# Kernel tuning notes

Hardware: AMD Instinct MI355X
Metric: run time of the kernel (lower is better)

The kernel has to match this reference:

```python
import jax, jax.numpy as jnp
import numpy as np

ORDER = 5
LOOKAHEAD = 0
NDF = 96  # n_df_bins


def setup_inputs() -> dict:
    key = jax.random.key(0)
    k1, k2, k3 = jax.random.split(key, 3)
    spec = jax.random.normal(k1, (16, 1, 2000, 481, 2), dtype=jnp.float32)
    coefs = jax.random.normal(k2, (16, 2000, ORDER, NDF, 2), dtype=jnp.float32)
    alpha = jax.random.uniform(k3, (16, 2000, 1), dtype=jnp.float32)
    return {"spec": spec, "coefs": coefs, "alpha": alpha}


def reference(spec, coefs, alpha):
    # spec: [B, 1, T, F, 2]; coefs: [B, T, ORDER, NDF, 2]; alpha: [B, T, 1]
    B, _, T, F, _ = spec.shape
    x = spec[:, 0, :, :NDF, :]  # [B, T, NDF, 2]
    # pad time axis: (order - lookahead - 1) before, lookahead after
    xp = jnp.pad(x, ((0, 0), (ORDER - LOOKAHEAD - 1, LOOKAHEAD), (0, 0), (0, 0)))
    # overlapping time windows of length ORDER (loop over small fixed tap count)
    w = jnp.stack([xp[:, k:k + T] for k in range(ORDER)], axis=2)  # [B, T, ORDER, NDF, 2]
    # complex multiply-accumulate per tap, then sum over taps
    re = w[..., 0] * coefs[..., 0] - w[..., 1] * coefs[..., 1]
    im = w[..., 1] * coefs[..., 0] + w[..., 0] * coefs[..., 1]
    spec_f = jnp.stack((re, im), axis=-1).sum(axis=2)  # [B, T, NDF, 2]
    # alpha blend on the low df_bins, copy the rest unchanged
    a = alpha.reshape(B, 1, T, 1, 1)
    mixed = spec_f[:, None] * a + spec[..., :NDF, :] * (1.0 - a)
    return spec.at[..., :NDF, :].set(mixed)
```

## Files before the change

### kernel.cpp

```cpp
#include <hip/hip_runtime.h>

#define BB 16
#define TT 2000
#define FF 481
#define NDF_ 96
#define ORDER_ 5
#define ROW_F 962
#define COEF_ROW_F 960

typedef float floatx4 __attribute__((ext_vector_type(4)));

__global__ __launch_bounds__(256) void copy_kernel(
    const floatx4* __restrict__ src, floatx4* __restrict__ dst, int n4)
{
    int idx    = blockIdx.x * 256 + threadIdx.x;
    int stride = gridDim.x * 256;
    for (int i = idx; i < n4; i += stride) {
        floatx4 v = __builtin_nontemporal_load(&src[i]);
        __builtin_nontemporal_store(v, &dst[i]);
    }
}

__global__ __launch_bounds__(768) void df_kernel(
    const float* __restrict__ spec,
    const float* __restrict__ coefs,
    const float* __restrict__ alpha,
    float* __restrict__ out)
{
    const int b  = blockIdx.x / 250;
    const int t0 = (blockIdx.x - b * 250) * 8;
    const int r  = threadIdx.x / 96;
    const int f  = threadIdx.x - r * 96;
    const int t  = t0 + r;
    const int bt = b * TT + t;

    const float a   = alpha[bt];
    const float oma = 1.0f - a;

    float acc_re = 0.0f, acc_im = 0.0f;
    const float2* cbase = (const float2*)(coefs + (long)bt * COEF_ROW_F + f * 2);
    #pragma unroll
    for (int k = 0; k < ORDER_; ++k) {
        const int tk = t - (ORDER_ - 1) + k;
        float2 x = make_float2(0.0f, 0.0f);
        if (tk >= 0) {
            x = *(const float2*)(spec + ((long)b * TT + tk) * ROW_F + f * 2);
        }
        const float2 c = cbase[k * NDF_];
        acc_re += x.x * c.x - x.y * c.y;
        acc_im += x.y * c.x + x.x * c.y;
    }

    const long row = (long)bt * ROW_F;
    const float2 s = *(const float2*)(spec + row + f * 2);
    float2 o;
    o.x = acc_re * a + s.x * oma;
    o.y = acc_im * a + s.y * oma;
    *(float2*)(out + row + f * 2) = o;
}

extern "C" void kernel_launch(void* const* d_in, const int* in_sizes, int n_in,
                              void* d_out, int out_size, void* d_ws, size_t ws_size,
                              hipStream_t stream) {
    const float* spec  = (const float*)d_in[0];
    const float* coefs = (const float*)d_in[1];
    const float* alpha = (const float*)d_in[2];
    float* out = (float*)d_out;

    const int n4 = (BB * TT * FF * 2) / 4;
    copy_kernel<<<8192, 256, 0, stream>>>((const floatx4*)spec, (floatx4*)out, n4);

    df_kernel<<<BB * 250, 768, 0, stream>>>(spec, coefs, alpha, out);
}
```

Before: 300.9 us.

## Stage spec time window in LDS and batch copy-kernel loads

The filter kernel now loads the 12-row spec window for each block into shared memory once. All five taps and the blend term are then read from LDS instead of making repeated global loads per thread. Separately, the copy kernel is restructured so each thread issues four independent 16-byte loads before its stores. Its grid is resized so that a single pass covers the whole tensor, and the copy loads drop the nontemporal hint. The cost is a __syncthreads and some LDS use per block.

```diff
diff --git a/kernel.cpp b/kernel.cpp
--- a/kernel.cpp
+++ b/kernel.cpp
@@ -13,13 +13,26 @@
 __global__ __launch_bounds__(256) void copy_kernel(
     const floatx4* __restrict__ src, floatx4* __restrict__ dst, int n4)
 {
-    int idx    = blockIdx.x * 256 + threadIdx.x;
-    int stride = gridDim.x * 256;
-    for (int i = idx; i < n4; i += stride) {
-        floatx4 v = __builtin_nontemporal_load(&src[i]);
-        __builtin_nontemporal_store(v, &dst[i]);
-    }
+    const int S = gridDim.x * 256;
+    int i = blockIdx.x * 256 + threadIdx.x;
+
+    const int i0 = i, i1 = i + S, i2 = i + 2 * S, i3 = i + 3 * S;
+    floatx4 v0, v1, v2, v3;
+    bool b0 = i0 < n4, b1 = i1 < n4, b2 = i2 < n4, b3 = i3 < n4;
+    if (b0) v0 = src[i0];
+    if (b1) v1 = src[i1];
+    if (b2) v2 = src[i2];
+    if (b3) v3 = src[i3];
+    if (b0) __builtin_nontemporal_store(v0, &dst[i0]);
+    if (b1) __builtin_nontemporal_store(v1, &dst[i1]);
+    if (b2) __builtin_nontemporal_store(v2, &dst[i2]);
+    if (b3) __builtin_nontemporal_store(v3, &dst[i3]);
 }
+
+#define ROWS_PER_BLK 8
+#define LDS_ROWS (ROWS_PER_BLK + ORDER_ - 1)
+#define LDS_F2_PER_ROW NDF_
+#define LDS_F2_TOTAL (LDS_ROWS * LDS_F2_PER_ROW)
 
 __global__ __launch_bounds__(768) void df_kernel(
     const float* __restrict__ spec,
@@ -27,10 +40,26 @@
     const float* __restrict__ alpha,
     float* __restrict__ out)
 {
-    const int b  = blockIdx.x / 250;
-    const int t0 = (blockIdx.x - b * 250) * 8;
-    const int r  = threadIdx.x / 96;
-    const int f  = threadIdx.x - r * 96;
+    __shared__ float2 xs[LDS_F2_TOTAL];
+
+    const int b  = blockIdx.x / (TT / ROWS_PER_BLK);
+    const int t0 = (blockIdx.x - b * (TT / ROWS_PER_BLK)) * ROWS_PER_BLK;
+    const int tid = threadIdx.x;
+
+    for (int j = tid; j < LDS_F2_TOTAL; j += 768) {
+        const int jr  = j / LDS_F2_PER_ROW;
+        const int jc  = j - jr * LDS_F2_PER_ROW;
+        const int t   = t0 - (ORDER_ - 1) + jr;
+        float2 v = make_float2(0.0f, 0.0f);
+        if (t >= 0) {
+            v = *(const float2*)(spec + ((long)b * TT + t) * ROW_F + jc * 2);
+        }
+        xs[j] = v;
+    }
+    __syncthreads();
+
+    const int r  = tid / NDF_;
+    const int f  = tid - r * NDF_;
     const int t  = t0 + r;
     const int bt = b * TT + t;
 
@@ -41,22 +70,17 @@
     const float2* cbase = (const float2*)(coefs + (long)bt * COEF_ROW_F + f * 2);
     #pragma unroll
     for (int k = 0; k < ORDER_; ++k) {
-        const int tk = t - (ORDER_ - 1) + k;
-        float2 x = make_float2(0.0f, 0.0f);
-        if (tk >= 0) {
-            x = *(const float2*)(spec + ((long)b * TT + tk) * ROW_F + f * 2);
-        }
+        const float2 x = xs[(r + k) * LDS_F2_PER_ROW + f];
         const float2 c = cbase[k * NDF_];
         acc_re += x.x * c.x - x.y * c.y;
         acc_im += x.y * c.x + x.x * c.y;
     }
 
-    const long row = (long)bt * ROW_F;
-    const float2 s = *(const float2*)(spec + row + f * 2);
+    const float2 s = xs[(r + ORDER_ - 1) * LDS_F2_PER_ROW + f];
     float2 o;
     o.x = acc_re * a + s.x * oma;
     o.y = acc_im * a + s.y * oma;
-    *(float2*)(out + row + f * 2) = o;
+    *(float2*)(out + (long)bt * ROW_F + f * 2) = o;
 }
 
 extern "C" void kernel_launch(void* const* d_in, const int* in_sizes, int n_in,
@@ -68,7 +92,7 @@
     float* out = (float*)d_out;
 
     const int n4 = (BB * TT * FF * 2) / 4;
-    copy_kernel<<<8192, 256, 0, stream>>>((const floatx4*)spec, (floatx4*)out, n4);
+    copy_kernel<<<7516, 256, 0, stream>>>((const floatx4*)spec, (floatx4*)out, n4);
 
-    df_kernel<<<BB * 250, 768, 0, stream>>>(spec, coefs, alpha, out);
+    df_kernel<<<BB * (TT / ROWS_PER_BLK), 768, 0, stream>>>(spec, coefs, alpha, out);
 }
```

Result: no change. 303.6 us (+0.9%).
